# Performance work log

Hardware: AMD Instinct MI355X
Metric: run time of the kernel (lower is better)

The kernel has to match this reference:

```python
import jax, jax.numpy as jnp
import numpy as np

B, T, C, H = 4, 2048, 1024, 16
D = C // H  # head dim = 64


def setup_inputs() -> dict:
    key = jax.random.key(0)
    ks = jax.random.split(key, 5)
    s = 1.0 / np.sqrt(C)
    return {
        "x": jax.random.normal(ks[0], (B, T, C), jnp.float32),
        "Wq": jax.random.normal(ks[1], (C, C), jnp.float32) * s,
        "bq": jnp.zeros((C,), jnp.float32),
        "Wk": jax.random.normal(ks[2], (C, C), jnp.float32) * s,
        "bk": jnp.zeros((C,), jnp.float32),
        "Wv": jax.random.normal(ks[3], (C, C), jnp.float32) * s,
        "bv": jnp.zeros((C,), jnp.float32),
        "Wp": jax.random.normal(ks[4], (C, C), jnp.float32) * s,
        "bp": jnp.zeros((C,), jnp.float32),
    }


def reference(x, Wq, bq, Wk, bk, Wv, bv, Wp, bp):
    # linear projections -> [B, H, T, D]
    def heads(t):
        return t.reshape(B, T, H, D).transpose(0, 2, 1, 3)
    q = heads(x @ Wq.T + bq)
    k = heads(x @ Wk.T + bk)
    v = heads(x @ Wv.T + bv)
    scale = 1.0 / np.sqrt(D)
    att = jnp.einsum("bhtd,bhsd->bhts", q, k) * scale  # [B,H,T,T]
    causal = jnp.tril(jnp.ones((T, T), bool))
    att = jnp.where(causal[None, None], att, -jnp.inf)
    att = jax.nn.softmax(att, axis=-1)
    y = jnp.einsum("bhts,bhsd->bhtd", att, v)  # [B,H,T,D]
    y = y.transpose(0, 2, 1, 3).reshape(B, T, C)
    return y @ Wp.T + bp
```

## Files before the change

### kernel.cpp

```cpp
#include <hip/hip_runtime.h>

typedef float f32x4 __attribute__((ext_vector_type(4)));
typedef float f32x16 __attribute__((ext_vector_type(16)));
typedef __bf16 bf16x8 __attribute__((ext_vector_type(8)));
typedef unsigned short u16x8 __attribute__((ext_vector_type(8)));

#define SCQ 0.1803368801111183f

__device__ inline unsigned short f2bf(float f) {
  unsigned int u = __builtin_bit_cast(unsigned int, f);
  u += 0x7FFFu + ((u >> 16) & 1u);
  return (unsigned short)(u >> 16);
}
__device__ inline unsigned short f2bf_fast(float f) {
  unsigned int u = __builtin_bit_cast(unsigned int, f);
  return (unsigned short)((u + 0x8000u) >> 16);
}

__device__ inline float fexp2(float x) {
#if __has_builtin(__builtin_amdgcn_exp2f)
  return __builtin_amdgcn_exp2f(x);
#else
  return exp2f(x);
#endif
}

template <int N>
__device__ inline float rowror(float v) {
  return __builtin_bit_cast(float, __builtin_amdgcn_update_dpp(
      0, __builtin_bit_cast(int, v), 0x120 | N, 0xF, 0xF, true));
}
__device__ inline float rowsum16(float v) {
  v += rowror<8>(v); v += rowror<4>(v);
  v += rowror<2>(v); v += rowror<1>(v);
  return v;
}

__device__ inline void gload_lds16(const unsigned short* g, unsigned short* l) {
  __builtin_amdgcn_global_load_lds(
      (const __attribute__((address_space(1))) unsigned int*)g,
      (__attribute__((address_space(3))) unsigned int*)l, 16, 0, 0);
}

__global__ void cvt_x(const float* __restrict__ in, unsigned short* __restrict__ out) {
  int i = (blockIdx.x * 256 + threadIdx.x) * 4;
  float4 f = *(const float4*)(in + i);
  ushort4 o;
  o.x = f2bf(f.x); o.y = f2bf(f.y); o.z = f2bf(f.z); o.w = f2bf(f.w);
  *(ushort4*)(out + i) = o;
}

__global__ void cvt_w(const float* __restrict__ a, const float* __restrict__ b,
                      const float* __restrict__ c, const float* __restrict__ d,
                      unsigned short* __restrict__ oa, unsigned short* __restrict__ ob,
                      unsigned short* __restrict__ oc, unsigned short* __restrict__ od) {
  const float* src[4] = {a, b, c, d};
  unsigned short* dst[4] = {oa, ob, oc, od};
  int m = blockIdx.y;
  int i = (blockIdx.x * 256 + threadIdx.x) * 4;
  float4 f = *(const float4*)(src[m] + i);
  ushort4 o;
  o.x = f2bf(f.x); o.y = f2bf(f.y); o.z = f2bf(f.z); o.w = f2bf(f.w);
  *(ushort4*)(dst[m] + i) = o;
}

template <int MODE>
__global__ __launch_bounds__(256) void gemm128(const unsigned short* __restrict__ A,
                                               const unsigned short* __restrict__ Bt,
                                               const float* __restrict__ b0,
                                               const float* __restrict__ b1,
                                               const float* __restrict__ b2,
                                               void* __restrict__ out,
                                               int M, int N, int K) {
  __shared__ __align__(16) unsigned short As[128 * 64];
  __shared__ __align__(16) unsigned short Bs[128 * 64];
  const int tid = threadIdx.x;
  const int lane = tid & 63, w = tid >> 6;
  const int l31 = lane & 31, half = lane >> 5;
  const int wm = w & 1, wn = w >> 1;
  const int m0 = blockIdx.x * 128, n0 = blockIdx.y * 128;

  f32x16 acc[2][2] = {};

  for (int kb = 0; kb < K; kb += 64) {
#pragma unroll
    for (int j = 0; j < 4; j++) {
      int ch = j * 256 + w * 64 + lane;
      int row = ch >> 3, pc = ch & 7;
      int c = pc ^ (row & 7);
      gload_lds16(A + (size_t)(m0 + row) * K + kb + c * 8, As + (size_t)(j * 256 + w * 64) * 8);
      gload_lds16(Bt + (size_t)(n0 + row) * K + kb + c * 8, Bs + (size_t)(j * 256 + w * 64) * 8);
    }
    __syncthreads();
#pragma unroll
    for (int ks = 0; ks < 64; ks += 16) {
      bf16x8 af[2], bfr[2];
#pragma unroll
      for (int at = 0; at < 2; at++) {
        int row = wm * 64 + at * 32 + l31;
        int pc = ((ks >> 3) + half) ^ (row & 7);
        af[at] = *(const bf16x8*)(As + row * 64 + pc * 8);
      }
#pragma unroll
      for (int nt = 0; nt < 2; nt++) {
        int row = wn * 64 + nt * 32 + l31;
        int pc = ((ks >> 3) + half) ^ (row & 7);
        bfr[nt] = *(const bf16x8*)(Bs + row * 64 + pc * 8);
      }
#pragma unroll
      for (int at = 0; at < 2; at++)
#pragma unroll
        for (int nt = 0; nt < 2; nt++)
          acc[at][nt] = __builtin_amdgcn_mfma_f32_32x32x16_bf16(af[at], bfr[nt], acc[at][nt], 0, 0, 0);
    }
    __syncthreads();
  }

#pragma unroll
  for (int at = 0; at < 2; at++)
#pragma unroll
    for (int nt = 0; nt < 2; nt++) {
      int col = n0 + wn * 64 + nt * 32 + l31;
      float bv, sc;
      int which = 0, cl = col;
      if (MODE == 0) {
        which = col >> 10; cl = col & 1023;
        const float* bp = (which == 0) ? b0 : ((which == 1) ? b1 : b2);
        bv = bp[cl];
        sc = (which == 0) ? SCQ : 1.f;
      } else {
        bv = b0[col]; sc = 1.f;
      }
#pragma unroll
      for (int reg = 0; reg < 16; reg++) {
        int row = m0 + wm * 64 + at * 32 + (reg & 3) + 8 * (reg >> 2) + 4 * half;
        float v = (acc[at][nt][reg] + bv) * sc;
        if (MODE == 0) {
          int h = cl >> 6, d = cl & 63;
          int b = row >> 11, t = row & 2047;
          ((unsigned short*)out)[(size_t)which * 8388608 +
                                 ((size_t)((b * 16 + h) * 2048 + t)) * 64 + d] = f2bf(v);
        } else {
          ((float*)out)[(size_t)row * N + col] = v;
        }
      }
    }
}

__global__ __launch_bounds__(256) void transpose_v(const unsigned short* __restrict__ V,
                                                   unsigned short* __restrict__ Vt) {
  constexpr int P = 66;
  __shared__ unsigned short L[64 * P];
  const int tid = threadIdx.x;
  const int bh = blockIdx.y;
  const int t0 = blockIdx.x * 64;
  const unsigned short* Vp = V + (size_t)bh * 2048 * 64;
  unsigned short* Op = Vt + (size_t)bh * 64 * 2048;
#pragma unroll
  for (int j = 0; j < 2; j++) {
    int r = (tid >> 3) + j * 32;
    int c = (tid & 7) * 8;
    u16x8 v = *(const u16x8*)(Vp + (size_t)(t0 + r) * 64 + c);
#pragma unroll
    for (int i = 0; i < 4; i++) {
      unsigned int pk = (unsigned int)v[2 * i] | ((unsigned int)v[2 * i + 1] << 16);
      *(unsigned int*)&L[r * P + c + 2 * i] = pk;
    }
  }
  __syncthreads();
#pragma unroll
  for (int j = 0; j < 2; j++) {
    int ch = j * 256 + tid;
    int d = ch >> 3, tc = (ch & 7) * 8;
    u16x8 o;
#pragma unroll
    for (int k = 0; k < 8; k++) o[k] = L[(tc + k) * P + d];
    *(u16x8*)(Op + (size_t)d * 2048 + t0 + tc) = o;
  }
}

__device__ __attribute__((always_inline)) inline
void attn_tile(int qt, int s0, const bf16x8* aq, const unsigned short* Ks,
               const unsigned short* Vs, unsigned short* pl,
               f32x4* o, float* lrow, int quad, int l15) {
  const bool full = (s0 + 63) <= qt;
  const int nsc = full ? 4 : (((qt + 15 - s0) >> 4) + 1);
  const int nsc2 = (nsc + 1) & ~1;
  const int pb = l15 >> 3, pp = l15 & 7;

#pragma unroll
  for (int sc = 0; sc < 4; sc++) {
    if (sc < nsc) {
      f32x4 s = {};
#pragma unroll
      for (int kh = 0; kh < 2; kh++) {
        int kr = sc * 16 + l15;
        int pc = (kh * 4 + quad) ^ (kr & 7);
        u16x8 bku = *(const u16x8*)(Ks + kr * 64 + pc * 8);
        s = __builtin_amdgcn_mfma_f32_16x16x32_bf16(aq[kh], __builtin_bit_cast(bf16x8, bku), s, 0, 0, 0);
      }
      if (full) {
#pragma unroll
        for (int r = 0; r < 4; r++) {
          float e = fexp2(s[r]);
          lrow[r] += e;
          int prow = quad * 4 + r;
          pl[prow * 64 + (((sc * 2 + pb) ^ (prow & 7)) << 3) + pp] = f2bf_fast(e);
        }
      } else {
        int sg = s0 + sc * 16 + l15;
#pragma unroll
        for (int r = 0; r < 4; r++) {
          float e = fexp2(s[r]);
          e = (sg > qt + quad * 4 + r) ? 0.f : e;
          lrow[r] += e;
          int prow = quad * 4 + r;
          pl[prow * 64 + (((sc * 2 + pb) ^ (prow & 7)) << 3) + pp] = f2bf_fast(e);
        }
      }
    } else if (sc < nsc2) {
#pragma unroll
      for (int r = 0; r < 4; r++) {
        int prow = quad * 4 + r;
        pl[prow * 64 + (((sc * 2 + pb) ^ (prow & 7)) << 3) + pp] = 0;
      }
    }
  }
  __asm__ __volatile__("" ::: "memory");
#pragma unroll
  for (int h2 = 0; h2 < 2; h2++) {
    if (h2 * 2 < nsc2) {
      u16x8 apu = *(const u16x8*)(pl + l15 * 64 + (((h2 * 4 + quad) ^ (l15 & 7)) << 3));
      bf16x8 ap = __builtin_bit_cast(bf16x8, apu);
#pragma unroll
      for (int dc = 0; dc < 4; dc++) {
        int vr = dc * 16 + l15;
        int pc = (h2 * 4 + quad) ^ (vr & 7);
        u16x8 vu = *(const u16x8*)(Vs + vr * 64 + pc * 8);
        o[dc] = __builtin_amdgcn_mfma_f32_16x16x32_bf16(ap, __builtin_bit_cast(bf16x8, vu), o[dc], 0, 0, 0);
      }
    }
  }
}

__global__ __launch_bounds__(256, 4) void attn_kernel(const unsigned short* __restrict__ Q,
                                                      const unsigned short* __restrict__ Km,
                                                      const unsigned short* __restrict__ Vt,
                                                      unsigned short* __restrict__ Y) {
  constexpr int T = 2048, D = 64;
  __shared__ __align__(16) unsigned short Ks[2][64 * 64];
  __shared__ __align__(16) unsigned short Vs[2][64 * 64];
  __shared__ __align__(16) unsigned short P_lds[4][16 * 64];
  const int tid = threadIdx.x;
  const int lane = tid & 63, w = tid >> 6;
  const int quad = lane >> 4, l15 = lane & 15;
  const int bh = blockIdx.x;
  const int b = bh >> 4, h = bh & 15;
  const int p = blockIdx.y;
  const unsigned short* Qp = Q + (size_t)bh * T * D;
  const unsigned short* Kp = Km + (size_t)bh * T * D;
  const unsigned short* Vp = Vt + (size_t)bh * D * T;
  unsigned short* pl = P_lds[w];

  const int bch0 = (w * 2) * 64, bch1 = (w * 2 + 1) * 64;
  const int ch0 = bch0 + lane, ch1 = bch1 + lane;
  const int row0 = ch0 >> 3, c0 = (ch0 & 7) ^ (row0 & 7);
  const int row1 = ch1 >> 3, c1 = (ch1 & 7) ^ (row1 & 7);

  for (int phase = 0; phase < 2; ++phase) {
    const int jt = phase ? (127 - (p * 4 + w)) : (p * 4 + w);
    const int qt = jt * 16;
    const int nit = phase ? (32 - p) : (p + 1);

    bf16x8 aq[2];
    aq[0] = *(const bf16x8*)(Qp + (size_t)(qt + l15) * D + quad * 8);
    aq[1] = *(const bf16x8*)(Qp + (size_t)(qt + l15) * D + 32 + quad * 8);
    __asm__ __volatile__("" :: "v"(__builtin_bit_cast(f32x4, aq[0])),
                              "v"(__builtin_bit_cast(f32x4, aq[1])));

    f32x4 o[4] = {};
    float lrow[4] = {0.f, 0.f, 0.f, 0.f};

    gload_lds16(Kp + (size_t)row0 * 64 + c0 * 8, Ks[0] + bch0 * 8);
    gload_lds16(Kp + (size_t)row1 * 64 + c1 * 8, Ks[0] + bch1 * 8);
    gload_lds16(Vp + (size_t)row0 * T + c0 * 8, Vs[0] + bch0 * 8);
    gload_lds16(Vp + (size_t)row1 * T + c1 * 8, Vs[0] + bch1 * 8);

    int cur = 0;
    for (int it = 0; it < nit; ++it) {
      const int s0 = it * 64;
      if (it + 1 < nit) {
        const int s1 = s0 + 64;
        unsigned short* kd = Ks[cur ^ 1];
        unsigned short* vd = Vs[cur ^ 1];
        gload_lds16(Kp + (size_t)(s1 + row0) * 64 + c0 * 8, kd + bch0 * 8);
        gload_lds16(Kp + (size_t)(s1 + row1) * 64 + c1 * 8, kd + bch1 * 8);
        gload_lds16(Vp + (size_t)row0 * T + s1 + c0 * 8, vd + bch0 * 8);
        gload_lds16(Vp + (size_t)row1 * T + s1 + c1 * 8, vd + bch1 * 8);
        __asm__ __volatile__("s_waitcnt vmcnt(4)" ::: "memory");
      } else {
        __asm__ __volatile__("s_waitcnt vmcnt(0)" ::: "memory");
      }
      __builtin_amdgcn_s_barrier();
      __builtin_amdgcn_sched_barrier(0);

      attn_tile(qt, s0, aq, Ks[cur], Vs[cur], pl, o, lrow, quad, l15);

      __builtin_amdgcn_sched_barrier(0);
      __builtin_amdgcn_s_barrier();
      cur ^= 1;
    }

#pragma unroll
    for (int r = 0; r < 4; r++) {
      float inv = 1.f / rowsum16(lrow[r]);
      int qg = qt + quad * 4 + r;
#pragma unroll
      for (int dc = 0; dc < 4; dc++)
        Y[((size_t)(b * T + qg)) * 1024 + h * 64 + dc * 16 + l15] = f2bf(o[dc][r] * inv);
    }
  }
}

extern "C" void kernel_launch(void* const* d_in, const int* in_sizes, int n_in,
                              void* d_out, int out_size, void* d_ws, size_t ws_size,
                              hipStream_t stream) {
  const float* x  = (const float*)d_in[0];
  const float* Wq = (const float*)d_in[1];
  const float* bq = (const float*)d_in[2];
  const float* Wk = (const float*)d_in[3];
  const float* bk = (const float*)d_in[4];
  const float* Wv = (const float*)d_in[5];
  const float* bv = (const float*)d_in[6];
  const float* Wp = (const float*)d_in[7];
  const float* bp = (const float*)d_in[8];

  char* ws = (char*)d_ws;
  unsigned short* xb  = (unsigned short*)(ws + 0);
  unsigned short* wqb = (unsigned short*)(ws + 16777216);
  unsigned short* wkb = (unsigned short*)(ws + 18874368);
  unsigned short* wvb = (unsigned short*)(ws + 20971520);
  unsigned short* wpb = (unsigned short*)(ws + 23068672);
  unsigned short* Qb  = (unsigned short*)(ws + 25165824);
  unsigned short* Kb  = (unsigned short*)(ws + 41943040);
  unsigned short* Vb  = (unsigned short*)(ws + 58720256);
  unsigned short* Vtb = xb;
  unsigned short* Yb  = Vb;

  cvt_x<<<8192, 256, 0, stream>>>(x, xb);
  cvt_w<<<dim3(1024, 4), 256, 0, stream>>>(Wq, Wk, Wv, Wp, wqb, wkb, wvb, wpb);

  gemm128<0><<<dim3(64, 24), 256, 0, stream>>>(xb, wqb, bq, bk, bv, Qb, 8192, 3072, 1024);

  transpose_v<<<dim3(32, 64), 256, 0, stream>>>(Vb, Vtb);
  attn_kernel<<<dim3(64, 16), 256, 0, stream>>>(Qb, Kb, Vtb, Yb);

  gemm128<1><<<dim3(64, 8), 256, 0, stream>>>(Yb, wpb, bp, bp, bp, d_out, 8192, 1024, 1024);
}
```

Measured before the change: 259.0 us.

## Rewrite attention core with 32x32 MFMA and register-resident P via permlane swap

The attention kernel now gives each wave 32 query rows instead of 16 and computes S^T and O^T with 32x32x16 bf16 MFMAs. The softmax probabilities are packed with v_cvt_pk_bf16 and rearranged in registers with v_permlane32_swap, so the per-wave P LDS staging buffer and its round trip are gone. Row sums reduce with a single cross-half shuffle, and the output is stored as packed bf16 pairs. The grid halves to 8 query groups per head and launch bounds drop to 2 blocks per SIMD, trading occupancy for more registers and a larger per-wave tile.

```diff
diff --git a/kernel.cpp b/kernel.cpp
--- a/kernel.cpp
+++ b/kernel.cpp
@@ -4,6 +4,7 @@
 typedef float f32x16 __attribute__((ext_vector_type(16)));
 typedef __bf16 bf16x8 __attribute__((ext_vector_type(8)));
 typedef unsigned short u16x8 __attribute__((ext_vector_type(8)));
+typedef unsigned int u32x4 __attribute__((ext_vector_type(4)));
 
 #define SCQ 0.1803368801111183f
 
@@ -11,10 +12,6 @@
   unsigned int u = __builtin_bit_cast(unsigned int, f);
   u += 0x7FFFu + ((u >> 16) & 1u);
   return (unsigned short)(u >> 16);
-}
-__device__ inline unsigned short f2bf_fast(float f) {
-  unsigned int u = __builtin_bit_cast(unsigned int, f);
-  return (unsigned short)((u + 0x8000u) >> 16);
 }
 
 __device__ inline float fexp2(float x) {
@@ -25,15 +22,13 @@
 #endif
 }
 
-template <int N>
-__device__ inline float rowror(float v) {
-  return __builtin_bit_cast(float, __builtin_amdgcn_update_dpp(
-      0, __builtin_bit_cast(int, v), 0x120 | N, 0xF, 0xF, true));
-}
-__device__ inline float rowsum16(float v) {
-  v += rowror<8>(v); v += rowror<4>(v);
-  v += rowror<2>(v); v += rowror<1>(v);
-  return v;
+__device__ inline unsigned int cvtpk_bf16(float a, float b) {
+  unsigned int r;
+  __asm__("v_cvt_pk_bf16_f32 %0, %1, %2" : "=v"(r) : "v"(a), "v"(b));
+  return r;
+}
+__device__ inline void permswap32(unsigned int& a, unsigned int& b) {
+  __asm__("v_permlane32_swap_b32 %0, %1" : "+v"(a), "+v"(b));
 }
 
 __device__ inline void gload_lds16(const unsigned short* g, unsigned short* l) {
@@ -179,88 +174,22 @@
   }
 }
 
-__device__ __attribute__((always_inline)) inline
-void attn_tile(int qt, int s0, const bf16x8* aq, const unsigned short* Ks,
-               const unsigned short* Vs, unsigned short* pl,
-               f32x4* o, float* lrow, int quad, int l15) {
-  const bool full = (s0 + 63) <= qt;
-  const int nsc = full ? 4 : (((qt + 15 - s0) >> 4) + 1);
-  const int nsc2 = (nsc + 1) & ~1;
-  const int pb = l15 >> 3, pp = l15 & 7;
-
-#pragma unroll
-  for (int sc = 0; sc < 4; sc++) {
-    if (sc < nsc) {
-      f32x4 s = {};
-#pragma unroll
-      for (int kh = 0; kh < 2; kh++) {
-        int kr = sc * 16 + l15;
-        int pc = (kh * 4 + quad) ^ (kr & 7);
-        u16x8 bku = *(const u16x8*)(Ks + kr * 64 + pc * 8);
-        s = __builtin_amdgcn_mfma_f32_16x16x32_bf16(aq[kh], __builtin_bit_cast(bf16x8, bku), s, 0, 0, 0);
-      }
-      if (full) {
-#pragma unroll
-        for (int r = 0; r < 4; r++) {
-          float e = fexp2(s[r]);
-          lrow[r] += e;
-          int prow = quad * 4 + r;
-          pl[prow * 64 + (((sc * 2 + pb) ^ (prow & 7)) << 3) + pp] = f2bf_fast(e);
-        }
-      } else {
-        int sg = s0 + sc * 16 + l15;
-#pragma unroll
-        for (int r = 0; r < 4; r++) {
-          float e = fexp2(s[r]);
-          e = (sg > qt + quad * 4 + r) ? 0.f : e;
-          lrow[r] += e;
-          int prow = quad * 4 + r;
-          pl[prow * 64 + (((sc * 2 + pb) ^ (prow & 7)) << 3) + pp] = f2bf_fast(e);
-        }
-      }
-    } else if (sc < nsc2) {
-#pragma unroll
-      for (int r = 0; r < 4; r++) {
-        int prow = quad * 4 + r;
-        pl[prow * 64 + (((sc * 2 + pb) ^ (prow & 7)) << 3) + pp] = 0;
-      }
-    }
-  }
-  __asm__ __volatile__("" ::: "memory");
-#pragma unroll
-  for (int h2 = 0; h2 < 2; h2++) {
-    if (h2 * 2 < nsc2) {
-      u16x8 apu = *(const u16x8*)(pl + l15 * 64 + (((h2 * 4 + quad) ^ (l15 & 7)) << 3));
-      bf16x8 ap = __builtin_bit_cast(bf16x8, apu);
-#pragma unroll
-      for (int dc = 0; dc < 4; dc++) {
-        int vr = dc * 16 + l15;
-        int pc = (h2 * 4 + quad) ^ (vr & 7);
-        u16x8 vu = *(const u16x8*)(Vs + vr * 64 + pc * 8);
-        o[dc] = __builtin_amdgcn_mfma_f32_16x16x32_bf16(ap, __builtin_bit_cast(bf16x8, vu), o[dc], 0, 0, 0);
-      }
-    }
-  }
-}
-
-__global__ __launch_bounds__(256, 4) void attn_kernel(const unsigned short* __restrict__ Q,
+__global__ __launch_bounds__(256, 2) void attn_kernel(const unsigned short* __restrict__ Q,
                                                       const unsigned short* __restrict__ Km,
                                                       const unsigned short* __restrict__ Vt,
                                                       unsigned short* __restrict__ Y) {
   constexpr int T = 2048, D = 64;
   __shared__ __align__(16) unsigned short Ks[2][64 * 64];
   __shared__ __align__(16) unsigned short Vs[2][64 * 64];
-  __shared__ __align__(16) unsigned short P_lds[4][16 * 64];
   const int tid = threadIdx.x;
   const int lane = tid & 63, w = tid >> 6;
-  const int quad = lane >> 4, l15 = lane & 15;
+  const int l31 = lane & 31, half = lane >> 5;
   const int bh = blockIdx.x;
   const int b = bh >> 4, h = bh & 15;
   const int p = blockIdx.y;
   const unsigned short* Qp = Q + (size_t)bh * T * D;
   const unsigned short* Kp = Km + (size_t)bh * T * D;
   const unsigned short* Vp = Vt + (size_t)bh * D * T;
-  unsigned short* pl = P_lds[w];
 
   const int bch0 = (w * 2) * 64, bch1 = (w * 2 + 1) * 64;
   const int ch0 = bch0 + lane, ch1 = bch1 + lane;
@@ -268,18 +197,22 @@
   const int row1 = ch1 >> 3, c1 = (ch1 & 7) ^ (row1 & 7);
 
   for (int phase = 0; phase < 2; ++phase) {
-    const int jt = phase ? (127 - (p * 4 + w)) : (p * 4 + w);
-    const int qt = jt * 16;
-    const int nit = phase ? (32 - p) : (p + 1);
-
-    bf16x8 aq[2];
-    aq[0] = *(const bf16x8*)(Qp + (size_t)(qt + l15) * D + quad * 8);
-    aq[1] = *(const bf16x8*)(Qp + (size_t)(qt + l15) * D + 32 + quad * 8);
+    const int jt = phase ? (63 - (p * 4 + w)) : (p * 4 + w);
+    const int qt = jt * 32;
+    const int nit = phase ? (32 - 2 * p) : (2 * p + 2);
+    const int qg = qt + l31;
+
+    bf16x8 aq[4];
+#pragma unroll
+    for (int kc = 0; kc < 4; kc++)
+      aq[kc] = *(const bf16x8*)(Qp + (size_t)qg * D + kc * 16 + half * 8);
     __asm__ __volatile__("" :: "v"(__builtin_bit_cast(f32x4, aq[0])),
-                              "v"(__builtin_bit_cast(f32x4, aq[1])));
-
-    f32x4 o[4] = {};
-    float lrow[4] = {0.f, 0.f, 0.f, 0.f};
+                              "v"(__builtin_bit_cast(f32x4, aq[1])),
+                              "v"(__builtin_bit_cast(f32x4, aq[2])),
+                              "v"(__builtin_bit_cast(f32x4, aq[3])));
+
+    f32x16 o0 = {}, o1 = {};
+    float lsum = 0.f;
 
     gload_lds16(Kp + (size_t)row0 * 64 + c0 * 8, Ks[0] + bch0 * 8);
     gload_lds16(Kp + (size_t)row1 * 64 + c1 * 8, Ks[0] + bch1 * 8);
@@ -304,20 +237,96 @@
       __builtin_amdgcn_s_barrier();
       __builtin_amdgcn_sched_barrier(0);
 
-      attn_tile(qt, s0, aq, Ks[cur], Vs[cur], pl, o, lrow, quad, l15);
+      if (s0 <= qt + 31) {
+        const unsigned short* Kb_ = Ks[cur];
+        const unsigned short* Vb_ = Vs[cur];
+
+        f32x16 sacc0 = {}, sacc1 = {};
+#pragma unroll
+        for (int kc = 0; kc < 4; kc++) {
+          int kr0 = l31;
+          int cc0 = (kc * 2 + half) ^ (kr0 & 7);
+          u16x8 k0 = *(const u16x8*)(Kb_ + kr0 * 64 + cc0 * 8);
+          sacc0 = __builtin_amdgcn_mfma_f32_32x32x16_bf16(
+              __builtin_bit_cast(bf16x8, k0), aq[kc], sacc0, 0, 0, 0);
+          int kr1 = 32 + l31;
+          int cc1 = (kc * 2 + half) ^ (kr1 & 7);
+          u16x8 k1 = *(const u16x8*)(Kb_ + kr1 * 64 + cc1 * 8);
+          sacc1 = __builtin_amdgcn_mfma_f32_32x32x16_bf16(
+              __builtin_bit_cast(bf16x8, k1), aq[kc], sacc1, 0, 0, 0);
+        }
+
+        const bool full = (s0 + 63) <= qt;
+        float e0_[16], e1_[16];
+        if (full) {
+#pragma unroll
+          for (int r = 0; r < 16; r++) { e0_[r] = fexp2(sacc0[r]); lsum += e0_[r]; }
+#pragma unroll
+          for (int r = 0; r < 16; r++) { e1_[r] = fexp2(sacc1[r]); lsum += e1_[r]; }
+        } else {
+#pragma unroll
+          for (int r = 0; r < 16; r++) {
+            int sg = s0 + (r & 3) + 8 * (r >> 2) + 4 * half;
+            float ex = fexp2(sacc0[r]);
+            ex = (sg > qg) ? 0.f : ex;
+            e0_[r] = ex; lsum += ex;
+          }
+#pragma unroll
+          for (int r = 0; r < 16; r++) {
+            int sg = s0 + 32 + (r & 3) + 8 * (r >> 2) + 4 * half;
+            float ex = fexp2(sacc1[r]);
+            ex = (sg > qg) ? 0.f : ex;
+            e1_[r] = ex; lsum += ex;
+          }
+        }
+
+        bf16x8 pf[4];
+        auto pack2 = [&](const float* e_, int kbase) {
+#pragma unroll
+          for (int kl = 0; kl < 2; kl++) {
+            int base = kl * 8;
+            unsigned int a0 = cvtpk_bf16(e_[base + 0], e_[base + 1]);
+            unsigned int b0v = cvtpk_bf16(e_[base + 4], e_[base + 5]);
+            permswap32(a0, b0v);
+            unsigned int a1 = cvtpk_bf16(e_[base + 2], e_[base + 3]);
+            unsigned int b1v = cvtpk_bf16(e_[base + 6], e_[base + 7]);
+            permswap32(a1, b1v);
+            u32x4 t = {a0, a1, b0v, b1v};
+            pf[kbase + kl] = __builtin_bit_cast(bf16x8, t);
+          }
+        };
+        pack2(e0_, 0);
+        pack2(e1_, 2);
+
+#pragma unroll
+        for (int kc = 0; kc < 4; kc++) {
+          int vr0 = l31;
+          int cc0 = (kc * 2 + half) ^ (vr0 & 7);
+          u16x8 v0 = *(const u16x8*)(Vb_ + vr0 * 64 + cc0 * 8);
+          o0 = __builtin_amdgcn_mfma_f32_32x32x16_bf16(
+              __builtin_bit_cast(bf16x8, v0), pf[kc], o0, 0, 0, 0);
+          int vr1 = 32 + l31;
+          int cc1 = (kc * 2 + half) ^ (vr1 & 7);
+          u16x8 v1 = *(const u16x8*)(Vb_ + vr1 * 64 + cc1 * 8);
+          o1 = __builtin_amdgcn_mfma_f32_32x32x16_bf16(
+              __builtin_bit_cast(bf16x8, v1), pf[kc], o1, 0, 0, 0);
+        }
+      }
 
       __builtin_amdgcn_sched_barrier(0);
       __builtin_amdgcn_s_barrier();
       cur ^= 1;
     }
 
-#pragma unroll
-    for (int r = 0; r < 4; r++) {
-      float inv = 1.f / rowsum16(lrow[r]);
-      int qg = qt + quad * 4 + r;
-#pragma unroll
-      for (int dc = 0; dc < 4; dc++)
-        Y[((size_t)(b * T + qg)) * 1024 + h * 64 + dc * 16 + l15] = f2bf(o[dc][r] * inv);
+    float tot = lsum + __shfl_xor(lsum, 32);
+    float inv = 1.f / tot;
+    unsigned short* Yrow = Y + ((size_t)(b * T + qg)) * 1024 + h * 64;
+#pragma unroll
+    for (int rp = 0; rp < 8; rp++) {
+      int r = rp * 2;
+      int d = (r & 3) + 8 * (r >> 2) + 4 * half;
+      *(unsigned int*)(Yrow + d)      = cvtpk_bf16(o0[r] * inv, o0[r + 1] * inv);
+      *(unsigned int*)(Yrow + 32 + d) = cvtpk_bf16(o1[r] * inv, o1[r + 1] * inv);
     }
   }
 }
@@ -353,7 +362,7 @@
   gemm128<0><<<dim3(64, 24), 256, 0, stream>>>(xb, wqb, bq, bk, bv, Qb, 8192, 3072, 1024);
 
   transpose_v<<<dim3(32, 64), 256, 0, stream>>>(Vb, Vtb);
-  attn_kernel<<<dim3(64, 16), 256, 0, stream>>>(Qb, Kb, Vtb, Yb);
+  attn_kernel<<<dim3(64, 8), 256, 0, stream>>>(Qb, Kb, Vtb, Yb);
 
   gemm128<1><<<dim3(64, 8), 256, 0, stream>>>(Yb, wpb, bp, bp, bp, d_out, 8192, 1024, 1024);
 }
```

Result: faster. 249.0 us (-3.9%).
